# Kernel tuning notes

Hardware: AMD Instinct MI355X
Metric: run time of the kernel (lower is better)

The kernel has to match this reference:

```python
import jax, jax.numpy as jnp
import numpy as np


def _dct_1d(x):
    # cat(x, flip(x)) -> fft(norm='forward') -> first L bins -> |.| * sign(Re)
    L = x.shape[-1]
    arr = jnp.concatenate([x, jnp.flip(x, axis=-1)], axis=-1)  # [..., 2L]
    f = jnp.fft.fft(arr, norm='forward')[..., :L]
    return jnp.abs(f) * jnp.sign(f.real)


def _dct_2d(x):
    row = _dct_1d(x)
    col = _dct_1d(row.swapaxes(-1, -2))
    return col.swapaxes(-1, -2)


def setup_inputs() -> dict:
    key = jax.random.key(0)
    k1, k2, k3 = jax.random.split(key, 3)
    B, C, H, W = 16, 256, 64, 64
    r = 16
    ip = jax.random.normal(k1, (B, C, H, W), dtype=jnp.float32)
    w1 = jax.random.normal(k2, (C, C // r), dtype=jnp.float32) * (1.0 / np.sqrt(C))
    w2 = jax.random.normal(k3, (C // r, C), dtype=jnp.float32) * (1.0 / np.sqrt(C // r))
    return {"ip": ip, "w1": w1, "w2": w2}


def reference(ip, w1, w2):
    B, C, H, W = ip.shape
    dct = _dct_2d(ip)                                  # [B,C,H,W]
    top1 = jnp.max(dct.reshape(B, C, H * W), axis=-1)  # top-k(k=1) == max, [B,C]
    h = jax.nn.relu(top1 @ w1)                         # [B, C//r]
    weights = jax.nn.sigmoid(h @ w2)                   # [B, C]
    return ip * weights[:, :, None, None]
```

## Files before the change

### kernel.cpp

```cpp
#include <hip/hip_runtime.h>
#include <math.h>


#define S 72

typedef __attribute__((ext_vector_type(8))) short bf16x8;
typedef __attribute__((ext_vector_type(4))) float f32x4;

__device__ inline unsigned short f2bf(float x) {
    union { float f; unsigned u; } v; v.f = x;
    unsigned r = v.u + 0x7FFF + ((v.u >> 16) & 1);
    return (unsigned short)(r >> 16);
}

__global__ __launch_bounds__(256, 4) void dct_max_kernel(const float* __restrict__ ip,
                                                         float* __restrict__ top1) {
    __shared__ unsigned short Dbf[64 * S];
    __shared__ unsigned short Xbf[64 * S];
    __shared__ unsigned short Tbf[64 * S];
    __shared__ float red[4];

    const int t = threadIdx.x;

#pragma unroll
    for (int i = 0; i < 16; ++i) {
        int idx = i * 256 + t;
        int u = idx >> 6, h = idx & 63;
        int mm = (u * (2 * h + 1)) & 255;
        Dbf[u * S + h] = f2bf(cospif((float)mm * (1.0f / 128.0f)));
    }

    const int wv = t >> 6;
    const int l = t & 63;
    const int m = l & 15;
    const int q = l >> 4;
    const int arow = (16 * wv + m) * S + 8 * q;
    const int xh = t >> 4;
    const int xw0 = (4 * t) & 63;

    const int bc0 = blockIdx.x * 2;
    const float4* src4 = (const float4*)(ip + (size_t)bc0 * 4096);

    float4 xv[4];
#pragma unroll
    for (int i = 0; i < 4; ++i) xv[i] = src4[i * 256 + t];

    __syncthreads();
    const bf16x8 da0 = *(const bf16x8*)&Dbf[arow];
    const bf16x8 da1 = *(const bf16x8*)&Dbf[arow + 32];

    for (int s = 0; s < 2; ++s) {
#pragma unroll
        for (int i = 0; i < 4; ++i) {
            ushort4 p;
            p.x = f2bf(xv[i].x); p.y = f2bf(xv[i].y);
            p.z = f2bf(xv[i].z); p.w = f2bf(xv[i].w);
            *(ushort4*)&Xbf[(16 * i + xh) * S + xw0] = p;
        }
        __syncthreads();

        if (s < 1) {
            const float4* nsrc = src4 + (size_t)(s + 1) * 1024;
#pragma unroll
            for (int i = 0; i < 4; ++i) xv[i] = nsrc[i * 256 + t];
        }

        f32x4 acc[4];
#pragma unroll
        for (int tn = 0; tn < 4; ++tn) {
            const int brow = (16 * tn + m) * S + 8 * q;
            bf16x8 b0 = *(const bf16x8*)&Xbf[brow];
            bf16x8 b1 = *(const bf16x8*)&Xbf[brow + 32];
            f32x4 c = {0.0f, 0.0f, 0.0f, 0.0f};
            c = __builtin_amdgcn_mfma_f32_16x16x32_bf16(da0, b0, c, 0, 0, 0);
            c = __builtin_amdgcn_mfma_f32_16x16x32_bf16(da1, b1, c, 0, 0, 0);
            acc[tn] = c;
        }
#pragma unroll
        for (int tn = 0; tn < 4; ++tn)
#pragma unroll
            for (int reg = 0; reg < 4; ++reg)
                Tbf[(16 * wv + 4 * q + reg) * S + 16 * tn + m] = f2bf(acc[tn][reg]);
        __syncthreads();

        bf16x8 ta0 = *(const bf16x8*)&Tbf[arow];
        bf16x8 ta1 = *(const bf16x8*)&Tbf[arow + 32];
        float mx = -3.4e38f;
#pragma unroll
        for (int tn = 0; tn < 4; ++tn) {
            const int brow = (16 * tn + m) * S + 8 * q;
            bf16x8 b0 = *(const bf16x8*)&Dbf[brow];
            bf16x8 b1 = *(const bf16x8*)&Dbf[brow + 32];
            f32x4 c = {0.0f, 0.0f, 0.0f, 0.0f};
            c = __builtin_amdgcn_mfma_f32_16x16x32_bf16(ta0, b0, c, 0, 0, 0);
            c = __builtin_amdgcn_mfma_f32_16x16x32_bf16(ta1, b1, c, 0, 0, 0);
            mx = fmaxf(mx, fmaxf(fmaxf(c[0], c[1]), fmaxf(c[2], c[3])));
        }

#pragma unroll
        for (int off = 32; off > 0; off >>= 1) mx = fmaxf(mx, __shfl_down(mx, off, 64));
        if (l == 0) red[wv] = mx;
        __syncthreads();
        if (t == 0) {
            float M = fmaxf(fmaxf(red[0], red[1]), fmaxf(red[2], red[3]));
            top1[bc0 + s] = M * (1.0f / 4096.0f);
        }
    }
}

__global__ __launch_bounds__(256, 4) void scale_kernel(const float* __restrict__ ip,
                                                       const float* __restrict__ top1,
                                                       const float* __restrict__ w1,
                                                       const float* __restrict__ w2,
                                                       float* __restrict__ out) {
    __shared__ float h_s[16];
    __shared__ float w_s[2];
    const int t = threadIdx.x;
    const int bc0 = blockIdx.x * 2;
    const int b = bc0 >> 8, c0 = bc0 & 255;

    const f32x4* ip4 = (const f32x4*)ip + (size_t)bc0 * 1024;
    f32x4* out4 = (f32x4*)out + (size_t)bc0 * 1024;

    const int j = t >> 4, i = t & 15;
    float tvals[16], wvals[16];
#pragma unroll
    for (int k = 0; k < 16; ++k) {
        int cc = i + 16 * k;
        tvals[k] = top1[b * 256 + cc];
        wvals[k] = w1[cc * 16 + j];
    }
    f32x4 v[8];
#pragma unroll
    for (int s = 0; s < 2; ++s)
#pragma unroll
        for (int k = 0; k < 4; ++k) v[s * 4 + k] = ip4[(size_t)s * 1024 + k * 256 + t];

    float partial = 0.0f;
#pragma unroll
    for (int k = 0; k < 16; ++k) partial = fmaf(tvals[k], wvals[k], partial);
#pragma unroll
    for (int off = 8; off > 0; off >>= 1) partial += __shfl_xor(partial, off, 16);
    if (i == 0) h_s[j] = fmaxf(partial, 0.0f);
    __syncthreads();

    if (t < 32) {
        const int sc = t >> 4, jj = t & 15;
        float p2 = h_s[jj] * w2[jj * 256 + (c0 + sc)];
#pragma unroll
        for (int off = 8; off > 0; off >>= 1) p2 += __shfl_xor(p2, off, 16);
        if (jj == 0) w_s[sc] = 1.0f / (1.0f + __expf(-p2));
    }
    __syncthreads();

#pragma unroll
    for (int s = 0; s < 2; ++s) {
        const float wt = w_s[s];
#pragma unroll
        for (int k = 0; k < 4; ++k) {
            f32x4 r = v[s * 4 + k] * wt;
            __builtin_nontemporal_store(r, &out4[(size_t)s * 1024 + k * 256 + t]);
        }
    }
}

extern "C" void kernel_launch(void* const* d_in, const int* in_sizes, int n_in,
                              void* d_out, int out_size, void* d_ws, size_t ws_size,
                              hipStream_t stream) {
    const float* ip = (const float*)d_in[0];
    const float* w1 = (const float*)d_in[1];
    const float* w2 = (const float*)d_in[2];
    float* out = (float*)d_out;
    float* top1 = (float*)d_ws;

    dct_max_kernel<<<2048, 256, 0, stream>>>(ip, top1);
    scale_kernel<<<2048, 256, 0, stream>>>(ip, top1, w1, w2, out);
}
```

Baseline: 128.3 us.

## Hoist MLP into separate kernel and process four channels per DCT block

The per-block MLP recomputation in the scale kernel moves into a small 16-block kernel that writes per-channel sigmoid weights to workspace once. The scale kernel then only reads two weights and streams ip to out. Separately, the DCT kernel now handles four channels per block over 1024 blocks, which amortizes building the cosine table across more channels. The cost is an extra kernel launch and fewer DCT blocks, which lowers parallelism per launch.

```diff
diff --git a/kernel.cpp b/kernel.cpp
--- a/kernel.cpp
+++ b/kernel.cpp
@@ -38,7 +38,7 @@
     const int xh = t >> 4;
     const int xw0 = (4 * t) & 63;
 
-    const int bc0 = blockIdx.x * 2;
+    const int bc0 = blockIdx.x * 4;
     const float4* src4 = (const float4*)(ip + (size_t)bc0 * 4096);
 
     float4 xv[4];
@@ -49,7 +49,7 @@
     const bf16x8 da0 = *(const bf16x8*)&Dbf[arow];
     const bf16x8 da1 = *(const bf16x8*)&Dbf[arow + 32];
 
-    for (int s = 0; s < 2; ++s) {
+    for (int s = 0; s < 4; ++s) {
 #pragma unroll
         for (int i = 0; i < 4; ++i) {
             ushort4 p;
@@ -59,7 +59,7 @@
         }
         __syncthreads();
 
-        if (s < 1) {
+        if (s < 3) {
             const float4* nsrc = src4 + (size_t)(s + 1) * 1024;
 #pragma unroll
             for (int i = 0; i < 4; ++i) xv[i] = nsrc[i * 256 + t];
@@ -108,54 +108,53 @@
     }
 }
 
+__global__ __launch_bounds__(256, 4) void mlp_kernel(const float* __restrict__ top1,
+                                                     const float* __restrict__ w1,
+                                                     const float* __restrict__ w2,
+                                                     float* __restrict__ weights) {
+    __shared__ float h_s[16];
+    const int t = threadIdx.x;
+    const int b = blockIdx.x;
+
+    const int j = t >> 4, i = t & 15;
+    float partial = 0.0f;
+#pragma unroll
+    for (int k = 0; k < 16; ++k) {
+        int cc = i + 16 * k;
+        partial = fmaf(top1[b * 256 + cc], w1[cc * 16 + j], partial);
+    }
+#pragma unroll
+    for (int off = 8; off > 0; off >>= 1) partial += __shfl_xor(partial, off, 16);
+    if (i == 0) h_s[j] = fmaxf(partial, 0.0f);
+    __syncthreads();
+
+    float p2 = 0.0f;
+#pragma unroll
+    for (int jj = 0; jj < 16; ++jj) p2 = fmaf(h_s[jj], w2[jj * 256 + t], p2);
+    weights[b * 256 + t] = 1.0f / (1.0f + __expf(-p2));
+}
+
 __global__ __launch_bounds__(256, 4) void scale_kernel(const float* __restrict__ ip,
-                                                       const float* __restrict__ top1,
-                                                       const float* __restrict__ w1,
-                                                       const float* __restrict__ w2,
+                                                       const float* __restrict__ weights,
                                                        float* __restrict__ out) {
-    __shared__ float h_s[16];
-    __shared__ float w_s[2];
     const int t = threadIdx.x;
     const int bc0 = blockIdx.x * 2;
-    const int b = bc0 >> 8, c0 = bc0 & 255;
+
+    const float w0 = weights[bc0];
+    const float w1v = weights[bc0 + 1];
 
     const f32x4* ip4 = (const f32x4*)ip + (size_t)bc0 * 1024;
     f32x4* out4 = (f32x4*)out + (size_t)bc0 * 1024;
 
-    const int j = t >> 4, i = t & 15;
-    float tvals[16], wvals[16];
-#pragma unroll
-    for (int k = 0; k < 16; ++k) {
-        int cc = i + 16 * k;
-        tvals[k] = top1[b * 256 + cc];
-        wvals[k] = w1[cc * 16 + j];
-    }
     f32x4 v[8];
 #pragma unroll
     for (int s = 0; s < 2; ++s)
 #pragma unroll
         for (int k = 0; k < 4; ++k) v[s * 4 + k] = ip4[(size_t)s * 1024 + k * 256 + t];
 
-    float partial = 0.0f;
-#pragma unroll
-    for (int k = 0; k < 16; ++k) partial = fmaf(tvals[k], wvals[k], partial);
-#pragma unroll
-    for (int off = 8; off > 0; off >>= 1) partial += __shfl_xor(partial, off, 16);
-    if (i == 0) h_s[j] = fmaxf(partial, 0.0f);
-    __syncthreads();
-
-    if (t < 32) {
-        const int sc = t >> 4, jj = t & 15;
-        float p2 = h_s[jj] * w2[jj * 256 + (c0 + sc)];
-#pragma unroll
-        for (int off = 8; off > 0; off >>= 1) p2 += __shfl_xor(p2, off, 16);
-        if (jj == 0) w_s[sc] = 1.0f / (1.0f + __expf(-p2));
-    }
-    __syncthreads();
-
 #pragma unroll
     for (int s = 0; s < 2; ++s) {
-        const float wt = w_s[s];
+        const float wt = (s == 0) ? w0 : w1v;
 #pragma unroll
         for (int k = 0; k < 4; ++k) {
             f32x4 r = v[s * 4 + k] * wt;
@@ -172,7 +171,9 @@
     const float* w2 = (const float*)d_in[2];
     float* out = (float*)d_out;
     float* top1 = (float*)d_ws;
+    float* weights = (float*)d_ws + 4096;
 
-    dct_max_kernel<<<2048, 256, 0, stream>>>(ip, top1);
-    scale_kernel<<<2048, 256, 0, stream>>>(ip, top1, w1, w2, out);
+    dct_max_kernel<<<1024, 256, 0, stream>>>(ip, top1);
+    mlp_kernel<<<16, 256, 0, stream>>>(top1, w1, w2, weights);
+    scale_kernel<<<2048, 256, 0, stream>>>(ip, weights, out);
 }
```

New measurement: 129.6 us. No clear change (+1.0%).
